# Performance work log

Hardware: AMD Instinct MI355X
Metric: run time of the kernel (lower is better)

Reference implementation:

```python
import jax, jax.numpy as jnp
import numpy as np

N = 50000        # nodes
E = 800000       # edges (avg degree 16)
OBS = 128        # observation_dim
HID = 64         # hidden_dim (per head)
H1 = 4           # heads in conv1
ACT = 32         # action_dim
NEG_SLOPE = 0.2  # GATv2 default negative_slope


def setup_inputs() -> dict:
    key = jax.random.key(0)
    ks = jax.random.split(key, 10)
    s = 0.05
    x = jax.random.normal(ks[0], (N, OBS), jnp.float32)
    edge_index = jax.random.randint(ks[1], (2, E), 0, N, dtype=jnp.int32)
    # conv1: GATv2Conv(OBS -> HID, heads=4, concat=True)
    W1l = jax.random.normal(ks[2], (OBS, H1 * HID), jnp.float32) * s  # lin_l (source)
    W1r = jax.random.normal(ks[3], (OBS, H1 * HID), jnp.float32) * s  # lin_r (target)
    att1 = jax.random.normal(ks[4], (H1, HID), jnp.float32) * s
    b1 = jnp.zeros((H1 * HID,), jnp.float32)
    # conv2: GATv2Conv(H1*HID -> ACT, heads=1, concat=False)
    W2l = jax.random.normal(ks[5], (H1 * HID, ACT), jnp.float32) * s
    W2r = jax.random.normal(ks[6], (H1 * HID, ACT), jnp.float32) * s
    att2 = jax.random.normal(ks[7], (1, ACT), jnp.float32) * s
    b2 = jnp.zeros((ACT,), jnp.float32)
    return {"x": x, "edge_index": edge_index, "W1l": W1l, "W1r": W1r,
            "att1": att1, "b1": b1, "W2l": W2l, "W2r": W2r,
            "att2": att2, "b2": b2}


def gatv2_layer(x, Wl, Wr, att, bias, src, dst, heads, out_ch, concat):
    """PyG GATv2Conv (add_self_loops=False, share_weights=False)."""
    n = x.shape[0]
    xl = (x @ Wl).reshape(n, heads, out_ch)  # source transform
    xr = (x @ Wr).reshape(n, heads, out_ch)  # target transform
    e = xl[src] + xr[dst]                    # [E, H, C] gathered messages
    g = jnp.where(e > 0, e, NEG_SLOPE * e)   # LeakyReLU
    logits = jnp.einsum('ehc,hc->eh', g, att)  # [E, H]
    # segment softmax over incoming edges of each destination node
    m = jax.ops.segment_max(logits, dst, num_segments=n)      # [N, H]
    ex = jnp.exp(logits - m[dst])
    denom = jax.ops.segment_sum(ex, dst, num_segments=n)      # [N, H]
    alpha = ex / denom[dst]                                   # [E, H]
    out = jax.ops.segment_sum(xl[src] * alpha[:, :, None], dst, num_segments=n)
    out = out.reshape(n, heads * out_ch) if concat else out.mean(axis=1)
    return out + bias


def reference(x, edge_index, W1l, W1r, att1, b1, W2l, W2r, att2, b2):
    src, dst = edge_index[0], edge_index[1]
    h = jax.nn.relu(gatv2_layer(x, W1l, W1r, att1, b1, src, dst, H1, HID, True))
    out = gatv2_layer(h, W2l, W2r, att2, b2, src, dst, 1, ACT, False)
    return out
```

## Files before the change

### kernel.cpp

```cpp
#include <hip/hip_runtime.h>
#include <hip/hip_bf16.h>
#include <math.h>


#define OBS 128
#define HID 64
#define H1 4
#define C1 256
#define ACT 32
#define PAD 128
#define NEG_SLOPE 0.2f
#define LOG2E 1.4426950408889634f

typedef __attribute__((ext_vector_type(2))) _Float16 h2;
typedef __attribute__((ext_vector_type(8))) _Float16 half8;
typedef __attribute__((ext_vector_type(4))) float f32x4;

__device__ inline h2 bc_h2(unsigned u) { return __builtin_bit_cast(h2, u); }
__device__ inline unsigned bc_u(h2 v) { return __builtin_bit_cast(unsigned, v); }
__device__ inline h2 lrelu2(h2 e) {
  const h2 k = {(_Float16)NEG_SLOPE, (_Float16)NEG_SLOPE};
  return __builtin_elementwise_max(e, e * k);
}

__global__ void prep0(const float* __restrict__ W1l, const float* __restrict__ W1r,
                      const float* __restrict__ W2l, const float* __restrict__ W2r,
                      _Float16* __restrict__ W1t, _Float16* __restrict__ W2t,
                      int* __restrict__ cursor, int N) {
  int i = blockIdx.x * 256 + threadIdx.x;
  if (i < N) cursor[i] = 0;
  if (i < 512 * 128) {
    int n = i >> 7, k = i & 127;
    float v = (n < C1) ? W1l[k * C1 + n] : W1r[k * C1 + (n - C1)];
    W1t[i] = (_Float16)v;
  }
  int j = i - 512 * 128;
  if (j >= 0 && j < 64 * 256) {
    int n = j >> 8, c = j & 255;
    float v = (n < ACT) ? W2l[c * ACT + n] : W2r[c * ACT + (n - ACT)];
    W2t[j] = (_Float16)v;
  }
}

__global__ __launch_bounds__(256) void gemm1_csr(
    const float* __restrict__ xf,
    const _Float16* __restrict__ W1t,
    _Float16* __restrict__ XLh,
    _Float16* __restrict__ XRh,
    int M,
    const int* __restrict__ src, const int* __restrict__ dst,
    int* __restrict__ cursor, unsigned short* __restrict__ esrc_p,
    int E, int gemmBlocks) {
  const int LDK = 136;
  __shared__ _Float16 As[128 * 136];
  __shared__ _Float16 Bs[128 * 136];

  if ((int)blockIdx.x >= gemmBlocks) {
    int e = ((int)blockIdx.x - gemmBlocks) * 256 + threadIdx.x;
    if (e < E) {
      int d = dst[e];
      int slot = atomicAdd(&cursor[d], 1);
      if (slot < PAD) esrc_p[((size_t)d << 7) + slot] = (unsigned short)src[e];
    }
    return;
  }

  const int tid = threadIdx.x;
  const int lane = tid & 63;
  const int wid = tid >> 6;
  const int wm = (wid & 1) * 64, wn = (wid >> 1) * 64;
  const int rowBase = blockIdx.x * 128;
  const int l15 = lane & 15, lq = lane >> 4;

#pragma unroll
  for (int cc = 0; cc < 8; ++cc) {
    int q = cc * 256 + tid;
    int r = q >> 4;
    int kc = (q & 15) * 8;
    int grow = rowBase + r;
    float4 f0 = make_float4(0.f, 0.f, 0.f, 0.f), f1 = f0;
    if (grow < M) {
      f0 = *(const float4*)(xf + (size_t)grow * 128 + kc);
      f1 = *(const float4*)(xf + (size_t)grow * 128 + kc + 4);
    }
    h2 p0 = {(_Float16)f0.x, (_Float16)f0.y};
    h2 p1 = {(_Float16)f0.z, (_Float16)f0.w};
    h2 p2 = {(_Float16)f1.x, (_Float16)f1.y};
    h2 p3 = {(_Float16)f1.z, (_Float16)f1.w};
    *(int4*)(As + r * LDK + kc) = make_int4(bc_u(p0), bc_u(p1), bc_u(p2), bc_u(p3));
  }
#pragma unroll
  for (int cc = 0; cc < 8; ++cc) {
    int q = cc * 256 + tid;
    int r = q >> 4;
    int kc = (q & 15) * 8;
    *(int4*)(Bs + r * LDK + kc) = *(const int4*)(W1t + (size_t)r * 128 + kc);
  }
  __syncthreads();

  for (int cb = 0; cb < 4; ++cb) {
    f32x4 acc[4][4];
#pragma unroll
    for (int i = 0; i < 4; ++i)
#pragma unroll
      for (int j = 0; j < 4; ++j) acc[i][j] = (f32x4){0.f, 0.f, 0.f, 0.f};

#pragma unroll
    for (int ks = 0; ks < 4; ++ks) {
      half8 af[4], bf[4];
#pragma unroll
      for (int t = 0; t < 4; ++t) {
        af[t] = *(const half8*)(As + (wm + t * 16 + l15) * LDK + ks * 32 + lq * 8);
        bf[t] = *(const half8*)(Bs + (wn + t * 16 + l15) * LDK + ks * 32 + lq * 8);
      }
#pragma unroll
      for (int mt = 0; mt < 4; ++mt)
#pragma unroll
        for (int nt = 0; nt < 4; ++nt)
          acc[mt][nt] = __builtin_amdgcn_mfma_f32_16x16x32_f16(
              af[mt], bf[nt], acc[mt][nt], 0, 0, 0);
    }

    _Float16* outp = (cb < 2) ? XLh : XRh;
    int colBase = (cb & 1) * 128;
#pragma unroll
    for (int mt = 0; mt < 4; ++mt) {
#pragma unroll
      for (int r = 0; r < 4; ++r) {
        int row = rowBase + wm + mt * 16 + lq * 4 + r;
        if (row >= M) continue;
#pragma unroll
        for (int nt = 0; nt < 4; ++nt) {
          int col = colBase + wn + nt * 16 + l15;
          outp[(size_t)row * C1 + col] = (_Float16)acc[mt][nt][r];
        }
      }
    }

    if (cb < 3) {
      __syncthreads();
#pragma unroll
      for (int cc = 0; cc < 8; ++cc) {
        int q = cc * 256 + tid;
        int r = q >> 4;
        int kc = (q & 15) * 8;
        *(int4*)(Bs + r * LDK + kc) =
            *(const int4*)(W1t + (size_t)((cb + 1) * 128 + r) * 128 + kc);
      }
      __syncthreads();
    }
  }
}

__global__ __launch_bounds__(256) void gemm_mfma2(
    const _Float16* __restrict__ Hh,
    const _Float16* __restrict__ W2t,
    _Float16* __restrict__ H2h,
    int M) {
  const int LDK = 136;
  __shared__ _Float16 As[128 * 136];
  __shared__ _Float16 Bs[64 * 136];
  const int tid = threadIdx.x;
  const int lane = tid & 63;
  const int wid = tid >> 6;
  const int wm = (wid & 1) * 64, wn = (wid >> 1) * 32;
  const int rowBase = blockIdx.x * 128;

  f32x4 acc[4][2];
#pragma unroll
  for (int i = 0; i < 4; ++i)
#pragma unroll
    for (int j = 0; j < 2; ++j) acc[i][j] = (f32x4){0.f, 0.f, 0.f, 0.f};

  const int l15 = lane & 15, lq = lane >> 4;

  for (int kb = 0; kb < 256; kb += 128) {
#pragma unroll
    for (int cc = 0; cc < 8; ++cc) {
      int q = cc * 256 + tid;
      int r = q >> 4;
      int kc = (q & 15) * 8;
      int grow = rowBase + r;
      int4 av = make_int4(0, 0, 0, 0);
      if (grow < M) av = *(const int4*)(Hh + (size_t)grow * 256 + kb + kc);
      *(int4*)(As + r * LDK + kc) = av;
    }
#pragma unroll
    for (int cc = 0; cc < 4; ++cc) {
      int q = cc * 256 + tid;
      int r = q >> 4;
      int kc = (q & 15) * 8;
      *(int4*)(Bs + r * LDK + kc) = *(const int4*)(W2t + (size_t)r * 256 + kb + kc);
    }
    __syncthreads();

#pragma unroll
    for (int ks = 0; ks < 4; ++ks) {
      half8 af[4], bf[2];
#pragma unroll
      for (int t = 0; t < 4; ++t)
        af[t] = *(const half8*)(As + (wm + t * 16 + l15) * LDK + ks * 32 + lq * 8);
#pragma unroll
      for (int t = 0; t < 2; ++t)
        bf[t] = *(const half8*)(Bs + (wn + t * 16 + l15) * LDK + ks * 32 + lq * 8);
#pragma unroll
      for (int mt = 0; mt < 4; ++mt)
#pragma unroll
        for (int nt = 0; nt < 2; ++nt)
          acc[mt][nt] = __builtin_amdgcn_mfma_f32_16x16x32_f16(
              af[mt], bf[nt], acc[mt][nt], 0, 0, 0);
    }
    __syncthreads();
  }

#pragma unroll
  for (int mt = 0; mt < 4; ++mt) {
#pragma unroll
    for (int r = 0; r < 4; ++r) {
      int row = rowBase + wm + mt * 16 + lq * 4 + r;
      if (row >= M) continue;
#pragma unroll
      for (int nt = 0; nt < 2; ++nt) {
        int col = wn + nt * 16 + l15;
        H2h[(size_t)row * 64 + col] = (_Float16)acc[mt][nt][r];
      }
    }
  }
}

__global__ __launch_bounds__(256) void agg1(const _Float16* __restrict__ XLh,
                                            const _Float16* XRh,
                                            const float* __restrict__ att1,
                                            const float* __restrict__ b1,
                                            const int* __restrict__ degp,
                                            const unsigned short* __restrict__ esrc_p,
                                            _Float16* Hh, int n_nodes) {
  int wave = threadIdx.x >> 6;
  int lane = threadIdx.x & 63;
  int n = blockIdx.x * 4 + wave;
  if (n >= n_nodes) return;
  int sl = lane & 31;
  int half = lane >> 5;
  int c8 = sl * 8;

  const char* XLb = (const char*)XLh + c8 * 2;
  int4 xru = *(const int4*)((const char*)XRh + ((size_t)n << 9) + c8 * 2);
  h2 xr[4] = {bc_h2(xru.x), bc_h2(xru.y), bc_h2(xru.z), bc_h2(xru.w)};
  const float* ap = att1 + (c8 >> 6) * HID + (c8 & 63);
  float4 a0 = *(const float4*)ap;
  float4 a1 = *(const float4*)(ap + 4);
  h2 av[4] = {{(_Float16)(a0.x * LOG2E), (_Float16)(a0.y * LOG2E)},
              {(_Float16)(a0.z * LOG2E), (_Float16)(a0.w * LOG2E)},
              {(_Float16)(a1.x * LOG2E), (_Float16)(a1.y * LOG2E)},
              {(_Float16)(a1.z * LOG2E), (_Float16)(a1.w * LOG2E)}};

  int d = min(degp[n], PAD);
  const unsigned short* ep = esrc_p + ((size_t)n << 7);
  float l = 0.f;
  h2 acc[4];
#pragma unroll
  for (int k = 0; k < 4; ++k) acc[k] = (h2){(_Float16)0.f, (_Float16)0.f};

  int base = 0;
  for (; base + 16 <= d; base += 16) {
    int4 u[8];
#pragma unroll
    for (int t = 0; t < 8; ++t) {
      int s = ep[base + 2 * t + half];
      u[t] = *(const int4*)(XLb + ((size_t)s << 9));
    }
    float c[8];
#pragma unroll
    for (int t = 0; t < 8; ++t) {
      h2 xa = bc_h2(u[t].x), xb = bc_h2(u[t].y), xc = bc_h2(u[t].z), xd = bc_h2(u[t].w);
      float cc = __builtin_amdgcn_fdot2(lrelu2(xa + xr[0]), av[0], 0.f, false);
      cc = __builtin_amdgcn_fdot2(lrelu2(xb + xr[1]), av[1], cc, false);
      cc = __builtin_amdgcn_fdot2(lrelu2(xc + xr[2]), av[2], cc, false);
      cc = __builtin_amdgcn_fdot2(lrelu2(xd + xr[3]), av[3], cc, false);
      c[t] = cc;
    }
#pragma unroll
    for (int t = 0; t < 8; ++t) {
      c[t] += __shfl_xor(c[t], 1);
      c[t] += __shfl_xor(c[t], 2);
      c[t] += __shfl_xor(c[t], 4);
    }
#pragma unroll
    for (int t = 0; t < 8; ++t) {
      float p = __builtin_amdgcn_exp2f(c[t]);
      l += p;
      _Float16 ph = (_Float16)p;
      h2 w = {ph, ph};
      acc[0] = acc[0] + w * bc_h2(u[t].x);
      acc[1] = acc[1] + w * bc_h2(u[t].y);
      acc[2] = acc[2] + w * bc_h2(u[t].z);
      acc[3] = acc[3] + w * bc_h2(u[t].w);
    }
  }
  for (; base + 4 <= d; base += 4) {
    int s0 = ep[base + half];
    int s1 = ep[base + 2 + half];
    int4 u0 = *(const int4*)(XLb + ((size_t)s0 << 9));
    int4 u1 = *(const int4*)(XLb + ((size_t)s1 << 9));
    h2 x0[4] = {bc_h2(u0.x), bc_h2(u0.y), bc_h2(u0.z), bc_h2(u0.w)};
    h2 x1[4] = {bc_h2(u1.x), bc_h2(u1.y), bc_h2(u1.z), bc_h2(u1.w)};
    float c0 = 0.f, c1 = 0.f;
#pragma unroll
    for (int k = 0; k < 4; ++k) {
      c0 = __builtin_amdgcn_fdot2(lrelu2(x0[k] + xr[k]), av[k], c0, false);
      c1 = __builtin_amdgcn_fdot2(lrelu2(x1[k] + xr[k]), av[k], c1, false);
    }
    c0 += __shfl_xor(c0, 1); c1 += __shfl_xor(c1, 1);
    c0 += __shfl_xor(c0, 2); c1 += __shfl_xor(c1, 2);
    c0 += __shfl_xor(c0, 4); c1 += __shfl_xor(c1, 4);
    float p0 = __builtin_amdgcn_exp2f(c0);
    float p1 = __builtin_amdgcn_exp2f(c1);
    l += p0 + p1;
    _Float16 q0 = (_Float16)p0, q1 = (_Float16)p1;
    h2 w0 = {q0, q0}, w1 = {q1, q1};
#pragma unroll
    for (int k = 0; k < 4; ++k) acc[k] = acc[k] + w0 * x0[k] + w1 * x1[k];
  }
  if (base < d) {
    int e0 = base + half, e1 = base + 2 + half;
    bool v0 = e0 < d, v1 = e1 < d;
    int s0 = ep[v0 ? e0 : 0];
    int s1 = ep[v1 ? e1 : 0];
    int4 u0 = *(const int4*)(XLb + ((size_t)s0 << 9));
    int4 u1 = *(const int4*)(XLb + ((size_t)s1 << 9));
    h2 x0[4] = {bc_h2(u0.x), bc_h2(u0.y), bc_h2(u0.z), bc_h2(u0.w)};
    h2 x1[4] = {bc_h2(u1.x), bc_h2(u1.y), bc_h2(u1.z), bc_h2(u1.w)};
    float c0 = 0.f, c1 = 0.f;
#pragma unroll
    for (int k = 0; k < 4; ++k) {
      c0 = __builtin_amdgcn_fdot2(lrelu2(x0[k] + xr[k]), av[k], c0, false);
      c1 = __builtin_amdgcn_fdot2(lrelu2(x1[k] + xr[k]), av[k], c1, false);
    }
    c0 += __shfl_xor(c0, 1); c1 += __shfl_xor(c1, 1);
    c0 += __shfl_xor(c0, 2); c1 += __shfl_xor(c1, 2);
    c0 += __shfl_xor(c0, 4); c1 += __shfl_xor(c1, 4);
    float p0 = v0 ? __builtin_amdgcn_exp2f(c0) : 0.f;
    float p1 = v1 ? __builtin_amdgcn_exp2f(c1) : 0.f;
    l += p0 + p1;
    _Float16 q0 = (_Float16)p0, q1 = (_Float16)p1;
    h2 w0 = {q0, q0}, w1 = {q1, q1};
#pragma unroll
    for (int k = 0; k < 4; ++k) acc[k] = acc[k] + w0 * x0[k] + w1 * x1[k];
  }

  l += __shfl_xor(l, 32);
#pragma unroll
  for (int k = 0; k < 4; ++k) {
    unsigned o = __shfl_xor((int)bc_u(acc[k]), 32);
    acc[k] = acc[k] + bc_h2(o);
  }

  float inv = (d > 0) ? 1.f / l : 0.f;
  if (half == 0) {
    float4 b0 = *(const float4*)(b1 + c8);
    float4 b3 = *(const float4*)(b1 + c8 + 4);
    float o0 = fmaxf((float)acc[0][0] * inv + b0.x, 0.f);
    float o1 = fmaxf((float)acc[0][1] * inv + b0.y, 0.f);
    float o2 = fmaxf((float)acc[1][0] * inv + b0.z, 0.f);
    float o3 = fmaxf((float)acc[1][1] * inv + b0.w, 0.f);
    float o4 = fmaxf((float)acc[2][0] * inv + b3.x, 0.f);
    float o5 = fmaxf((float)acc[2][1] * inv + b3.y, 0.f);
    float o6 = fmaxf((float)acc[3][0] * inv + b3.z, 0.f);
    float o7 = fmaxf((float)acc[3][1] * inv + b3.w, 0.f);
    h2 q0 = {(_Float16)o0, (_Float16)o1};
    h2 q1 = {(_Float16)o2, (_Float16)o3};
    h2 q2 = {(_Float16)o4, (_Float16)o5};
    h2 q3 = {(_Float16)o6, (_Float16)o7};
    *(int4*)((char*)Hh + ((size_t)n << 9) + c8 * 2) =
        make_int4(bc_u(q0), bc_u(q1), bc_u(q2), bc_u(q3));
  }
}

__global__ __launch_bounds__(256) void agg2(const _Float16* __restrict__ H2h,
                                            const float* __restrict__ att2,
                                            const float* __restrict__ b2,
                                            const int* __restrict__ degp,
                                            const unsigned short* __restrict__ esrc_p,
                                            float* __restrict__ out, int n_nodes) {
  int wave = threadIdx.x >> 6;
  int lane = threadIdx.x & 63;
  int n = blockIdx.x * 4 + wave;
  if (n >= n_nodes) return;
  int g = lane >> 3;
  int j = lane & 7;
  int c4 = j * 4;

  const char* Hb = (const char*)H2h + c4 * 2;
  uint2 hru = *(const uint2*)((const char*)H2h + ((size_t)n << 7) + 64 + c4 * 2);
  h2 hr0 = bc_h2(hru.x), hr1 = bc_h2(hru.y);
  float4 af = *(const float4*)(att2 + c4);
  h2 a0 = {(_Float16)(af.x * LOG2E), (_Float16)(af.y * LOG2E)};
  h2 a1 = {(_Float16)(af.z * LOG2E), (_Float16)(af.w * LOG2E)};

  int d = min(degp[n], PAD);
  const unsigned short* ep = esrc_p + ((size_t)n << 7);
  float l = 0.f;
  h2 acc0 = {(_Float16)0.f, (_Float16)0.f}, acc1 = acc0;

  int base = 0;
  for (; base + 16 <= d; base += 16) {
    int s0 = ep[base + g];
    int s1 = ep[base + 8 + g];
    uint2 u0 = *(const uint2*)(Hb + ((size_t)s0 << 7));
    uint2 u1 = *(const uint2*)(Hb + ((size_t)s1 << 7));
    h2 h00 = bc_h2(u0.x), h01 = bc_h2(u0.y);
    h2 h10 = bc_h2(u1.x), h11 = bc_h2(u1.y);
    float c0 = __builtin_amdgcn_fdot2(lrelu2(h00 + hr0), a0,
               __builtin_amdgcn_fdot2(lrelu2(h01 + hr1), a1, 0.f, false), false);
    float c1 = __builtin_amdgcn_fdot2(lrelu2(h10 + hr0), a0,
               __builtin_amdgcn_fdot2(lrelu2(h11 + hr1), a1, 0.f, false), false);
    c0 += __shfl_xor(c0, 1); c1 += __shfl_xor(c1, 1);
    c0 += __shfl_xor(c0, 2); c1 += __shfl_xor(c1, 2);
    c0 += __shfl_xor(c0, 4); c1 += __shfl_xor(c1, 4);
    float p0 = __builtin_amdgcn_exp2f(c0);
    float p1 = __builtin_amdgcn_exp2f(c1);
    l += p0 + p1;
    _Float16 q0 = (_Float16)p0, q1 = (_Float16)p1;
    h2 w0 = {q0, q0}, w1 = {q1, q1};
    acc0 = acc0 + w0 * h00 + w1 * h10;
    acc1 = acc1 + w0 * h01 + w1 * h11;
  }
  for (; base + 8 <= d; base += 8) {
    int s = ep[base + g];
    uint2 u = *(const uint2*)(Hb + ((size_t)s << 7));
    h2 h0 = bc_h2(u.x), h1 = bc_h2(u.y);
    float c = __builtin_amdgcn_fdot2(lrelu2(h0 + hr0), a0,
              __builtin_amdgcn_fdot2(lrelu2(h1 + hr1), a1, 0.f, false), false);
    c += __shfl_xor(c, 1);
    c += __shfl_xor(c, 2);
    c += __shfl_xor(c, 4);
    float p = __builtin_amdgcn_exp2f(c);
    l += p;
    _Float16 ph = (_Float16)p;
    h2 p2 = {ph, ph};
    acc0 = acc0 + p2 * h0;
    acc1 = acc1 + p2 * h1;
  }
  if (base < d) {
    int e = base + g;
    bool v = e < d;
    int s = ep[v ? e : 0];
    uint2 u = *(const uint2*)(Hb + ((size_t)s << 7));
    h2 h0 = bc_h2(u.x), h1 = bc_h2(u.y);
    float c = __builtin_amdgcn_fdot2(lrelu2(h0 + hr0), a0,
              __builtin_amdgcn_fdot2(lrelu2(h1 + hr1), a1, 0.f, false), false);
    c += __shfl_xor(c, 1);
    c += __shfl_xor(c, 2);
    c += __shfl_xor(c, 4);
    float p = v ? __builtin_amdgcn_exp2f(c) : 0.f;
    l += p;
    _Float16 ph = (_Float16)p;
    h2 p2 = {ph, ph};
    acc0 = acc0 + p2 * h0;
    acc1 = acc1 + p2 * h1;
  }

#pragma unroll
  for (int o = 8; o < 64; o <<= 1) {
    l += __shfl_xor(l, o);
    acc0 = acc0 + bc_h2((unsigned)__shfl_xor((int)bc_u(acc0), o));
    acc1 = acc1 + bc_h2((unsigned)__shfl_xor((int)bc_u(acc1), o));
  }

  float inv = (d > 0) ? 1.f / l : 0.f;
  if (g == 0) {
    float4 bb = *(const float4*)(b2 + c4);
    float4 o;
    o.x = (float)acc0[0] * inv + bb.x;
    o.y = (float)acc0[1] * inv + bb.y;
    o.z = (float)acc1[0] * inv + bb.z;
    o.w = (float)acc1[1] * inv + bb.w;
    *(float4*)(out + (size_t)n * ACT + c4) = o;
  }
}

extern "C" void kernel_launch(void* const* d_in, const int* in_sizes, int n_in,
                              void* d_out, int out_size, void* d_ws, size_t ws_size,
                              hipStream_t stream) {
  (void)n_in; (void)out_size; (void)ws_size;
  const float* x    = (const float*)d_in[0];
  const int*   ei   = (const int*)d_in[1];
  const float* W1l  = (const float*)d_in[2];
  const float* W1r  = (const float*)d_in[3];
  const float* att1 = (const float*)d_in[4];
  const float* b1   = (const float*)d_in[5];
  const float* W2l  = (const float*)d_in[6];
  const float* W2r  = (const float*)d_in[7];
  const float* att2 = (const float*)d_in[8];
  const float* b2   = (const float*)d_in[9];
  float* out = (float*)d_out;

  const int N = in_sizes[0] / OBS;
  const int E = in_sizes[1] / 2;
  const int* src = ei;
  const int* dst = ei + E;

  _Float16* XLh = (_Float16*)d_ws;
  _Float16* XRh = XLh + (size_t)N * C1;
  _Float16* W1t = XRh + (size_t)N * C1;
  _Float16* W2t = W1t + 512 * 128;
  int* cursor   = (int*)(W2t + 64 * 256);
  unsigned short* esrc_p = (unsigned short*)(cursor + N);
  _Float16* Hh  = XRh;
  _Float16* H2h = XLh;

  dim3 b256(256);
  int csrBlocks = (E + 255) / 256;
  int gemmBlocks = (N + 127) / 128;
  int prepBlocks = (512 * 128 + 64 * 256 + 255) / 256;

  prep0<<<prepBlocks, b256, 0, stream>>>(W1l, W1r, W2l, W2r, W1t, W2t, cursor, N);
  gemm1_csr<<<gemmBlocks + csrBlocks, b256, 0, stream>>>(
      x, W1t, XLh, XRh, N, src, dst, cursor, esrc_p, E, gemmBlocks);
  agg1<<<(N + 3) / 4, b256, 0, stream>>>(XLh, XRh, att1, b1, cursor, esrc_p, Hh, N);
  gemm_mfma2<<<gemmBlocks, b256, 0, stream>>>(Hh, W2t, H2h, N);
  agg2<<<(N + 3) / 4, b256, 0, stream>>>(H2h, att2, b2, cursor, esrc_p, out, N);
}
```

Baseline: 226.2 us.

## Split CSR build from GEMM1 and process two nodes per wave in agg2

```diff
diff --git a/kernel.cpp b/kernel.cpp
--- a/kernel.cpp
+++ b/kernel.cpp
@@ -42,28 +42,28 @@
   }
 }
 
-__global__ __launch_bounds__(256) void gemm1_csr(
+__global__ __launch_bounds__(256) void csr_build(const int* __restrict__ src,
+                                                 const int* __restrict__ dst,
+                                                 int* __restrict__ cursor,
+                                                 unsigned short* __restrict__ esrc_p,
+                                                 int E) {
+  int e = blockIdx.x * 256 + threadIdx.x;
+  if (e < E) {
+    int d = dst[e];
+    int slot = atomicAdd(&cursor[d], 1);
+    if (slot < PAD) esrc_p[((size_t)d << 7) + slot] = (unsigned short)src[e];
+  }
+}
+
+__global__ __launch_bounds__(256) void gemm1(
     const float* __restrict__ xf,
     const _Float16* __restrict__ W1t,
     _Float16* __restrict__ XLh,
     _Float16* __restrict__ XRh,
-    int M,
-    const int* __restrict__ src, const int* __restrict__ dst,
-    int* __restrict__ cursor, unsigned short* __restrict__ esrc_p,
-    int E, int gemmBlocks) {
+    int M) {
   const int LDK = 136;
   __shared__ _Float16 As[128 * 136];
   __shared__ _Float16 Bs[128 * 136];
-
-  if ((int)blockIdx.x >= gemmBlocks) {
-    int e = ((int)blockIdx.x - gemmBlocks) * 256 + threadIdx.x;
-    if (e < E) {
-      int d = dst[e];
-      int slot = atomicAdd(&cursor[d], 1);
-      if (slot < PAD) esrc_p[((size_t)d << 7) + slot] = (unsigned short)src[e];
-    }
-    return;
-  }
 
   const int tid = threadIdx.x;
   const int lane = tid & 63;
@@ -384,98 +384,115 @@
                                             float* __restrict__ out, int n_nodes) {
   int wave = threadIdx.x >> 6;
   int lane = threadIdx.x & 63;
-  int n = blockIdx.x * 4 + wave;
-  if (n >= n_nodes) return;
+  int n0 = (blockIdx.x * 4 + wave) * 2;
+  if (n0 >= n_nodes) return;
+  int n1 = n0 + 1;
+  bool has1 = n1 < n_nodes;
+  int n1s = has1 ? n1 : n0;
   int g = lane >> 3;
   int j = lane & 7;
   int c4 = j * 4;
 
   const char* Hb = (const char*)H2h + c4 * 2;
-  uint2 hru = *(const uint2*)((const char*)H2h + ((size_t)n << 7) + 64 + c4 * 2);
-  h2 hr0 = bc_h2(hru.x), hr1 = bc_h2(hru.y);
+  uint2 hru0 = *(const uint2*)((const char*)H2h + ((size_t)n0 << 7) + 64 + c4 * 2);
+  uint2 hru1 = *(const uint2*)((const char*)H2h + ((size_t)n1s << 7) + 64 + c4 * 2);
+  h2 hr00 = bc_h2(hru0.x), hr01 = bc_h2(hru0.y);
+  h2 hr10 = bc_h2(hru1.x), hr11 = bc_h2(hru1.y);
   float4 af = *(const float4*)(att2 + c4);
   h2 a0 = {(_Float16)(af.x * LOG2E), (_Float16)(af.y * LOG2E)};
   h2 a1 = {(_Float16)(af.z * LOG2E), (_Float16)(af.w * LOG2E)};
 
-  int d = min(degp[n], PAD);
-  const unsigned short* ep = esrc_p + ((size_t)n << 7);
-  float l = 0.f;
-  h2 acc0 = {(_Float16)0.f, (_Float16)0.f}, acc1 = acc0;
-
-  int base = 0;
-  for (; base + 16 <= d; base += 16) {
-    int s0 = ep[base + g];
-    int s1 = ep[base + 8 + g];
-    uint2 u0 = *(const uint2*)(Hb + ((size_t)s0 << 7));
-    uint2 u1 = *(const uint2*)(Hb + ((size_t)s1 << 7));
-    h2 h00 = bc_h2(u0.x), h01 = bc_h2(u0.y);
-    h2 h10 = bc_h2(u1.x), h11 = bc_h2(u1.y);
-    float c0 = __builtin_amdgcn_fdot2(lrelu2(h00 + hr0), a0,
-               __builtin_amdgcn_fdot2(lrelu2(h01 + hr1), a1, 0.f, false), false);
-    float c1 = __builtin_amdgcn_fdot2(lrelu2(h10 + hr0), a0,
-               __builtin_amdgcn_fdot2(lrelu2(h11 + hr1), a1, 0.f, false), false);
-    c0 += __shfl_xor(c0, 1); c1 += __shfl_xor(c1, 1);
-    c0 += __shfl_xor(c0, 2); c1 += __shfl_xor(c1, 2);
-    c0 += __shfl_xor(c0, 4); c1 += __shfl_xor(c1, 4);
-    float p0 = __builtin_amdgcn_exp2f(c0);
-    float p1 = __builtin_amdgcn_exp2f(c1);
-    l += p0 + p1;
-    _Float16 q0 = (_Float16)p0, q1 = (_Float16)p1;
-    h2 w0 = {q0, q0}, w1 = {q1, q1};
-    acc0 = acc0 + w0 * h00 + w1 * h10;
-    acc1 = acc1 + w0 * h01 + w1 * h11;
-  }
-  for (; base + 8 <= d; base += 8) {
-    int s = ep[base + g];
-    uint2 u = *(const uint2*)(Hb + ((size_t)s << 7));
-    h2 h0 = bc_h2(u.x), h1 = bc_h2(u.y);
-    float c = __builtin_amdgcn_fdot2(lrelu2(h0 + hr0), a0,
-              __builtin_amdgcn_fdot2(lrelu2(h1 + hr1), a1, 0.f, false), false);
-    c += __shfl_xor(c, 1);
-    c += __shfl_xor(c, 2);
-    c += __shfl_xor(c, 4);
-    float p = __builtin_amdgcn_exp2f(c);
-    l += p;
-    _Float16 ph = (_Float16)p;
-    h2 p2 = {ph, ph};
-    acc0 = acc0 + p2 * h0;
-    acc1 = acc1 + p2 * h1;
-  }
-  if (base < d) {
-    int e = base + g;
-    bool v = e < d;
-    int s = ep[v ? e : 0];
-    uint2 u = *(const uint2*)(Hb + ((size_t)s << 7));
-    h2 h0 = bc_h2(u.x), h1 = bc_h2(u.y);
-    float c = __builtin_amdgcn_fdot2(lrelu2(h0 + hr0), a0,
-              __builtin_amdgcn_fdot2(lrelu2(h1 + hr1), a1, 0.f, false), false);
-    c += __shfl_xor(c, 1);
-    c += __shfl_xor(c, 2);
-    c += __shfl_xor(c, 4);
-    float p = v ? __builtin_amdgcn_exp2f(c) : 0.f;
-    l += p;
-    _Float16 ph = (_Float16)p;
-    h2 p2 = {ph, ph};
-    acc0 = acc0 + p2 * h0;
-    acc1 = acc1 + p2 * h1;
+  int d0 = min(degp[n0], PAD);
+  int d1 = has1 ? min(degp[n1], PAD) : 0;
+  const unsigned short* ep0 = esrc_p + ((size_t)n0 << 7);
+  const unsigned short* ep1 = esrc_p + ((size_t)n1s << 7);
+
+  float l0 = 0.f, l1 = 0.f;
+  h2 z = {(_Float16)0.f, (_Float16)0.f};
+  h2 acc00 = z, acc01 = z, acc10 = z, acc11 = z;
+
+  int dmax = d0 > d1 ? d0 : d1;
+  for (int base = 0; base < dmax; base += 16) {
+    int eA = base + g, eB = base + 8 + g;
+    bool vA0 = eA < d0, vB0 = eB < d0;
+    bool vA1 = eA < d1, vB1 = eB < d1;
+    int sA0 = ep0[vA0 ? eA : 0];
+    int sB0 = ep0[vB0 ? eB : 0];
+    int sA1 = ep1[vA1 ? eA : 0];
+    int sB1 = ep1[vB1 ? eB : 0];
+    uint2 uA0 = *(const uint2*)(Hb + ((size_t)sA0 << 7));
+    uint2 uB0 = *(const uint2*)(Hb + ((size_t)sB0 << 7));
+    uint2 uA1 = *(const uint2*)(Hb + ((size_t)sA1 << 7));
+    uint2 uB1 = *(const uint2*)(Hb + ((size_t)sB1 << 7));
+    h2 hA0x = bc_h2(uA0.x), hA0y = bc_h2(uA0.y);
+    h2 hB0x = bc_h2(uB0.x), hB0y = bc_h2(uB0.y);
+    h2 hA1x = bc_h2(uA1.x), hA1y = bc_h2(uA1.y);
+    h2 hB1x = bc_h2(uB1.x), hB1y = bc_h2(uB1.y);
+    float cA0 = __builtin_amdgcn_fdot2(lrelu2(hA0x + hr00), a0,
+                __builtin_amdgcn_fdot2(lrelu2(hA0y + hr01), a1, 0.f, false), false);
+    float cB0 = __builtin_amdgcn_fdot2(lrelu2(hB0x + hr00), a0,
+                __builtin_amdgcn_fdot2(lrelu2(hB0y + hr01), a1, 0.f, false), false);
+    float cA1 = __builtin_amdgcn_fdot2(lrelu2(hA1x + hr10), a0,
+                __builtin_amdgcn_fdot2(lrelu2(hA1y + hr11), a1, 0.f, false), false);
+    float cB1 = __builtin_amdgcn_fdot2(lrelu2(hB1x + hr10), a0,
+                __builtin_amdgcn_fdot2(lrelu2(hB1y + hr11), a1, 0.f, false), false);
+#pragma unroll
+    for (int o = 1; o < 8; o <<= 1) {
+      cA0 += __shfl_xor(cA0, o); cB0 += __shfl_xor(cB0, o);
+      cA1 += __shfl_xor(cA1, o); cB1 += __shfl_xor(cB1, o);
+    }
+    float pA0 = vA0 ? __builtin_amdgcn_exp2f(cA0) : 0.f;
+    float pB0 = vB0 ? __builtin_amdgcn_exp2f(cB0) : 0.f;
+    float pA1 = vA1 ? __builtin_amdgcn_exp2f(cA1) : 0.f;
+    float pB1 = vB1 ? __builtin_amdgcn_exp2f(cB1) : 0.f;
+    l0 += pA0 + pB0;
+    l1 += pA1 + pB1;
+    _Float16 qA0 = (_Float16)pA0, qB0 = (_Float16)pB0;
+    _Float16 qA1 = (_Float16)pA1, qB1 = (_Float16)pB1;
+    h2 wA0 = {qA0, qA0}, wB0 = {qB0, qB0};
+    h2 wA1 = {qA1, qA1}, wB1 = {qB1, qB1};
+    acc00 = acc00 + wA0 * hA0x + wB0 * hB0x;
+    acc01 = acc01 + wA0 * hA0y + wB0 * hB0y;
+    acc10 = acc10 + wA1 * hA1x + wB1 * hB1x;
+    acc11 = acc11 + wA1 * hA1y + wB1 * hB1y;
   }
 
 #pragma unroll
   for (int o = 8; o < 64; o <<= 1) {
-    l += __shfl_xor(l, o);
-    acc0 = acc0 + bc_h2((unsigned)__shfl_xor((int)bc_u(acc0), o));
-    acc1 = acc1 + bc_h2((unsigned)__shfl_xor((int)bc_u(acc1), o));
-  }
-
-  float inv = (d > 0) ? 1.f / l : 0.f;
+    l0 += __shfl_xor(l0, o);
+    l1 += __shfl_xor(l1, o);
+    acc00 = acc00 + bc_h2((unsigned)__shfl_xor((int)bc_u(acc00), o));
+    acc01 = acc01 + bc_h2((unsigned)__shfl_xor((int)bc_u(acc01), o));
+    acc10 = acc10 + bc_h2((unsigned)__shfl_xor((int)bc_u(acc10), o));
+    acc11 = acc11 + bc_h2((unsigned)__shfl_xor((int)bc_u(acc11), o));
+  }
+
   if (g == 0) {
     float4 bb = *(const float4*)(b2 + c4);
     float4 o;
-    o.x = (float)acc0[0] * inv + bb.x;
-    o.y = (float)acc0[1] * inv + bb.y;
-    o.z = (float)acc1[0] * inv + bb.z;
-    o.w = (float)acc1[1] * inv + bb.w;
-    *(float4*)(out + (size_t)n * ACT + c4) = o;
+    if (d0 > 0) {
+      float inv = 1.f / l0;
+      o.x = (float)acc00[0] * inv + bb.x;
+      o.y = (float)acc00[1] * inv + bb.y;
+      o.z = (float)acc01[0] * inv + bb.z;
+      o.w = (float)acc01[1] * inv + bb.w;
+    } else {
+      o = bb;
+    }
+    *(float4*)(out + (size_t)n0 * ACT + c4) = o;
+  } else if (g == 1 && has1) {
+    float4 bb = *(const float4*)(b2 + c4);
+    float4 o;
+    if (d1 > 0) {
+      float inv = 1.f / l1;
+      o.x = (float)acc10[0] * inv + bb.x;
+      o.y = (float)acc10[1] * inv + bb.y;
+      o.z = (float)acc11[0] * inv + bb.z;
+      o.w = (float)acc11[1] * inv + bb.w;
+    } else {
+      o = bb;
+    }
+    *(float4*)(out + (size_t)n1 * ACT + c4) = o;
   }
 }
 
@@ -515,9 +532,9 @@
   int prepBlocks = (512 * 128 + 64 * 256 + 255) / 256;
 
   prep0<<<prepBlocks, b256, 0, stream>>>(W1l, W1r, W2l, W2r, W1t, W2t, cursor, N);
-  gemm1_csr<<<gemmBlocks + csrBlocks, b256, 0, stream>>>(
-      x, W1t, XLh, XRh, N, src, dst, cursor, esrc_p, E, gemmBlocks);
+  csr_build<<<csrBlocks, b256, 0, stream>>>(src, dst, cursor, esrc_p, E);
+  gemm1<<<gemmBlocks, b256, 0, stream>>>(x, W1t, XLh, XRh, N);
   agg1<<<(N + 3) / 4, b256, 0, stream>>>(XLh, XRh, att1, b1, cursor, esrc_p, Hh, N);
   gemm_mfma2<<<gemmBlocks, b256, 0, stream>>>(Hh, W2t, H2h, N);
-  agg2<<<(N + 3) / 4, b256, 0, stream>>>(H2h, att2, b2, cursor, esrc_p, out, N);
-}
+  agg2<<<(N + 7) / 8, b256, 0, stream>>>(H2h, att2, b2, cursor, esrc_p, out, N);
+}
```

Result: slower. 246.4 us (+8.9%).

## Fold CSR scatter into every GEMM1 block instead of separate scatter blocks

Applied to the files above, without the earlier changes.

```diff
diff --git a/kernel.cpp b/kernel.cpp
--- a/kernel.cpp
+++ b/kernel.cpp
@@ -42,7 +42,7 @@
   }
 }
 
-__global__ __launch_bounds__(256) void gemm1_csr(
+__global__ __launch_bounds__(256) void gemm1_sc(
     const float* __restrict__ xf,
     const _Float16* __restrict__ W1t,
     _Float16* __restrict__ XLh,
@@ -50,22 +50,36 @@
     int M,
     const int* __restrict__ src, const int* __restrict__ dst,
     int* __restrict__ cursor, unsigned short* __restrict__ esrc_p,
-    int E, int gemmBlocks) {
+    int E, int ept) {
   const int LDK = 136;
   __shared__ _Float16 As[128 * 136];
   __shared__ _Float16 Bs[128 * 136];
 
-  if ((int)blockIdx.x >= gemmBlocks) {
-    int e = ((int)blockIdx.x - gemmBlocks) * 256 + threadIdx.x;
-    if (e < E) {
-      int d = dst[e];
-      int slot = atomicAdd(&cursor[d], 1);
-      if (slot < PAD) esrc_p[((size_t)d << 7) + slot] = (unsigned short)src[e];
-    }
-    return;
-  }
-
   const int tid = threadIdx.x;
+
+  {
+    int base = blockIdx.x * ept * 256;
+    for (int b0 = 0; b0 < ept; b0 += 8) {
+      int ee[8], dd[8], ssv[8];
+#pragma unroll
+      for (int r = 0; r < 8; ++r) {
+        int e = base + (b0 + r) * 256 + tid;
+        ee[r] = e;
+        int ec = (e < E) ? e : 0;
+        dd[r] = dst[ec];
+        ssv[r] = src[ec];
+      }
+      int slot[8];
+#pragma unroll
+      for (int r = 0; r < 8; ++r)
+        slot[r] = (ee[r] < E) ? atomicAdd(&cursor[dd[r]], 1) : PAD;
+#pragma unroll
+      for (int r = 0; r < 8; ++r)
+        if (ee[r] < E && slot[r] < PAD)
+          esrc_p[((size_t)dd[r] << 7) + slot[r]] = (unsigned short)ssv[r];
+    }
+  }
+
   const int lane = tid & 63;
   const int wid = tid >> 6;
   const int wm = (wid & 1) * 64, wn = (wid >> 1) * 64;
@@ -510,13 +524,14 @@
   _Float16* H2h = XLh;
 
   dim3 b256(256);
-  int csrBlocks = (E + 255) / 256;
   int gemmBlocks = (N + 127) / 128;
   int prepBlocks = (512 * 128 + 64 * 256 + 255) / 256;
+  int ept = (E + gemmBlocks * 256 - 1) / (gemmBlocks * 256);
+  ept = (ept + 7) & ~7;
 
   prep0<<<prepBlocks, b256, 0, stream>>>(W1l, W1r, W2l, W2r, W1t, W2t, cursor, N);
-  gemm1_csr<<<gemmBlocks + csrBlocks, b256, 0, stream>>>(
-      x, W1t, XLh, XRh, N, src, dst, cursor, esrc_p, E, gemmBlocks);
+  gemm1_sc<<<gemmBlocks, b256, 0, stream>>>(
+      x, W1t, XLh, XRh, N, src, dst, cursor, esrc_p, E, ept);
   agg1<<<(N + 3) / 4, b256, 0, stream>>>(XLh, XRh, att1, b1, cursor, esrc_p, Hh, N);
   gemm_mfma2<<<gemmBlocks, b256, 0, stream>>>(Hh, W2t, H2h, N);
   agg2<<<(N + 3) / 4, b256, 0, stream>>>(H2h, att2, b2, cursor, esrc_p, out, N);
```

Measured after the change: 240.4 us. 6.3% more time.

## Build padded CSR via two-level bucket sort instead of global atomics

Applied to the files above, without the earlier changes.

```diff
diff --git a/kernel.cpp b/kernel.cpp
--- a/kernel.cpp
+++ b/kernel.cpp
@@ -11,6 +11,7 @@
 #define PAD 128
 #define NEG_SLOPE 0.2f
 #define LOG2E 1.4426950408889634f
+#define SB 512
 
 typedef __attribute__((ext_vector_type(2))) _Float16 h2;
 typedef __attribute__((ext_vector_type(8))) _Float16 half8;
@@ -42,28 +43,123 @@
   }
 }
 
-__global__ __launch_bounds__(256) void gemm1_csr(
+__global__ __launch_bounds__(256) void hist_k(const int* __restrict__ dst,
+                                              unsigned* __restrict__ cntG,
+                                              int E, int epb) {
+  __shared__ unsigned cnt[256];
+  int t = threadIdx.x;
+  cnt[t] = 0;
+  __syncthreads();
+  int beg = blockIdx.x * epb;
+  int end = beg + epb;
+  if (end > E) end = E;
+  for (int e = beg + t; e < end; e += 256) {
+    int b = dst[e] >> 8;
+    atomicAdd(&cnt[b], 1u);
+  }
+  __syncthreads();
+  cntG[blockIdx.x * 256 + t] = cnt[t];
+}
+
+__global__ __launch_bounds__(256) void scanB_k(unsigned* __restrict__ cntG,
+                                               unsigned* __restrict__ totals) {
+  __shared__ unsigned s[256];
+  int b = blockIdx.x;
+  int t = threadIdx.x;
+  unsigned c0 = cntG[(2 * t) * 256 + b];
+  unsigned c1 = cntG[(2 * t + 1) * 256 + b];
+  s[t] = c0 + c1;
+  __syncthreads();
+#pragma unroll
+  for (int off = 1; off < 256; off <<= 1) {
+    unsigned tmp = 0;
+    if (t >= off) tmp = s[t - off];
+    __syncthreads();
+    if (t >= off) s[t] += tmp;
+    __syncthreads();
+  }
+  unsigned excl = s[t] - (c0 + c1);
+  cntG[(2 * t) * 256 + b] = excl;
+  cntG[(2 * t + 1) * 256 + b] = excl + c0;
+  if (t == 255) totals[b] = s[255];
+}
+
+__global__ __launch_bounds__(256) void scanT_k(const unsigned* __restrict__ totals,
+                                               unsigned* __restrict__ bases) {
+  __shared__ unsigned s[256];
+  int t = threadIdx.x;
+  unsigned v = totals[t];
+  s[t] = v;
+  __syncthreads();
+#pragma unroll
+  for (int off = 1; off < 256; off <<= 1) {
+    unsigned tmp = 0;
+    if (t >= off) tmp = s[t - off];
+    __syncthreads();
+    if (t >= off) s[t] += tmp;
+    __syncthreads();
+  }
+  bases[t] = s[t] - v;
+}
+
+__global__ __launch_bounds__(256) void scat_k(const int* __restrict__ src,
+                                              const int* __restrict__ dst,
+                                              const unsigned* __restrict__ cntG,
+                                              const unsigned* __restrict__ bases,
+                                              unsigned* __restrict__ sorted,
+                                              int E, int epb) {
+  __shared__ unsigned lbase[256];
+  __shared__ unsigned lrank[256];
+  int t = threadIdx.x;
+  lbase[t] = bases[t] + cntG[blockIdx.x * 256 + t];
+  lrank[t] = 0;
+  __syncthreads();
+  int beg = blockIdx.x * epb;
+  int end = beg + epb;
+  if (end > E) end = E;
+  for (int e = beg + t; e < end; e += 256) {
+    int d = dst[e];
+    int sv = src[e];
+    int b = d >> 8;
+    unsigned r = atomicAdd(&lrank[b], 1u);
+    sorted[lbase[b] + r] = ((unsigned)(d & 255) << 16) | (unsigned)sv;
+  }
+}
+
+__global__ __launch_bounds__(256) void bcsr_k(const unsigned* __restrict__ sorted,
+                                              const unsigned* __restrict__ bases,
+                                              const unsigned* __restrict__ totals,
+                                              unsigned short* __restrict__ esrc_p,
+                                              int* __restrict__ cursor, int N) {
+  __shared__ unsigned cnt2[256];
+  int b = blockIdx.x;
+  int t = threadIdx.x;
+  cnt2[t] = 0;
+  __syncthreads();
+  unsigned beg = bases[b];
+  unsigned end = beg + totals[b];
+  for (unsigned e = beg + t; e < end; e += 256) {
+    unsigned u = sorted[e];
+    int dl = u >> 16;
+    unsigned short sv = (unsigned short)(u & 0xFFFFu);
+    unsigned slot = atomicAdd(&cnt2[dl], 1u);
+    if (slot < PAD)
+      esrc_p[((size_t)((b << 8) + dl) << 7) + slot] = sv;
+  }
+  __syncthreads();
+  int node = (b << 8) + t;
+  if (node < N) cursor[node] = (int)cnt2[t];
+}
+
+__global__ __launch_bounds__(256) void gemm1(
     const float* __restrict__ xf,
     const _Float16* __restrict__ W1t,
     _Float16* __restrict__ XLh,
     _Float16* __restrict__ XRh,
-    int M,
-    const int* __restrict__ src, const int* __restrict__ dst,
-    int* __restrict__ cursor, unsigned short* __restrict__ esrc_p,
-    int E, int gemmBlocks) {
+    int M) {
   const int LDK = 136;
   __shared__ _Float16 As[128 * 136];
   __shared__ _Float16 Bs[128 * 136];
-
-  if ((int)blockIdx.x >= gemmBlocks) {
-    int e = ((int)blockIdx.x - gemmBlocks) * 256 + threadIdx.x;
-    if (e < E) {
-      int d = dst[e];
-      int slot = atomicAdd(&cursor[d], 1);
-      if (slot < PAD) esrc_p[((size_t)d << 7) + slot] = (unsigned short)src[e];
-    }
-    return;
-  }
 
   const int tid = threadIdx.x;
   const int lane = tid & 63;
@@ -509,14 +605,23 @@
   _Float16* Hh  = XRh;
   _Float16* H2h = XLh;
 
+  unsigned* sortedW = (unsigned*)d_ws;
+  unsigned* cntG    = sortedW + E;
+  unsigned* totals  = cntG + SB * 256;
+  unsigned* bases   = totals + 256;
+
   dim3 b256(256);
-  int csrBlocks = (E + 255) / 256;
   int gemmBlocks = (N + 127) / 128;
   int prepBlocks = (512 * 128 + 64 * 256 + 255) / 256;
+  int epb = (E + SB - 1) / SB;
 
   prep0<<<prepBlocks, b256, 0, stream>>>(W1l, W1r, W2l, W2r, W1t, W2t, cursor, N);
-  gemm1_csr<<<gemmBlocks + csrBlocks, b256, 0, stream>>>(
-      x, W1t, XLh, XRh, N, src, dst, cursor, esrc_p, E, gemmBlocks);
+  hist_k<<<SB, b256, 0, stream>>>(dst, cntG, E, epb);
+  scanB_k<<<256, b256, 0, stream>>>(cntG, totals);
+  scanT_k<<<1, b256, 0, stream>>>(totals, bases);
+  scat_k<<<SB, b256, 0, stream>>>(src, dst, cntG, bases, sortedW, E, epb);
+  bcsr_k<<<256, b256, 0, stream>>>(sortedW, bases, totals, esrc_p, cursor, N);
+  gemm1<<<gemmBlocks, b256, 0, stream>>>(x, W1t, XLh, XRh, N);
   agg1<<<(N + 3) / 4, b256, 0, stream>>>(XLh, XRh, att1, b1, cursor, esrc_p, Hh, N);
   gemm_mfma2<<<gemmBlocks, b256, 0, stream>>>(Hh, W2t, H2h, N);
   agg2<<<(N + 3) / 4, b256, 0, stream>>>(H2h, att2, b2, cursor, esrc_p, out, N);
```

Measured after the change: 229.0 us. About the same (+1.2%).
